# Kernel optimization log

Measured on AMD Instinct MI355X. Metric: run time of the kernel, lower is better.

## Reference

```python
import jax, jax.numpy as jnp
import numpy as np

B, N, D = 64, 4096, 512
ATT = 128


def setup_inputs() -> dict:
    key = jax.random.key(0)
    ks = jax.random.split(key, 7)
    s = lambda fan_in: 1.0 / np.sqrt(fan_in)
    return {
        "v_I": jax.random.normal(ks[0], (B, N, D), dtype=jnp.float32),
        "v_Q": jax.random.normal(ks[1], (B, D), dtype=jnp.float32),
        "W_I": jax.random.normal(ks[2], (D, ATT), dtype=jnp.float32) * s(D),
        "W_Q": jax.random.normal(ks[3], (D, ATT), dtype=jnp.float32) * s(D),
        "b_Q": jnp.zeros((ATT,), dtype=jnp.float32),
        "W_p": jax.random.normal(ks[4], (ATT, 1), dtype=jnp.float32) * s(ATT),
        "b_p": jnp.zeros((1,), dtype=jnp.float32),
    }


def reference(v_I, v_Q, W_I, W_Q, b_Q, W_p, b_p):
    # v_I: [B, N, D], v_Q: [B, D]
    v_I_att = jnp.tanh(jnp.einsum("bnd,da->bna", v_I, W_I))          # [B, N, A]
    v_Q_att = jnp.tanh(v_Q @ W_Q + b_Q)[:, None, :]                  # [B, 1, A]
    h_A = jnp.tanh(v_I_att + v_Q_att)                                # [B, N, A]
    # dropout is identity in inference/reference mode
    p_I = (jnp.einsum("bna,ao->bno", h_A, W_p) + b_p)[..., 0]        # [B, N]
    p_I_output = jax.nn.softmax(p_I, axis=-1)                        # [B, N]
    v_att = jnp.einsum("bn,bnd->bd", p_I_output, v_I)                # [B, D]
    u = v_att + v_Q                                                  # [B, D]
    return (p_I_output, u)
```

## Files before the change

### kernel.cpp

```cpp
#include <hip/hip_runtime.h>
#include <cstdint>
#include <cstddef>

#define B_ 64
#define N_ 4096
#define D_ 512
#define A_ 128
#define BK 64

typedef unsigned short u16;
typedef __attribute__((ext_vector_type(8))) short bf16x8;
typedef __attribute__((ext_vector_type(4))) float f32x4;

__device__ __forceinline__ u16 cvt_bf16(float x) {
    unsigned u = __float_as_uint(x);
    return (u16)((u + 0x7FFFu + ((u >> 16) & 1u)) >> 16);
}
__device__ __forceinline__ unsigned pack2_bf16(float a, float b) {
    unsigned ua = __float_as_uint(a), ub = __float_as_uint(b);
    unsigned ra = (ua + 0x7FFFu + ((ua >> 16) & 1u)) >> 16;
    unsigned rb = (ub + 0x7FFFu + ((ub >> 16) & 1u)) >> 16;
    return ra | (rb << 16);
}
__device__ __forceinline__ float fast_tanh(float x) {
    float ax = fabsf(x);
    float e  = __expf(-2.0f * ax);
    float r  = __fdividef(1.0f - e, 1.0f + e);
    return x < 0.0f ? -r : r;
}
__device__ __forceinline__ void gl_lds16(const void* g, void* l) {
    __builtin_amdgcn_global_load_lds(
        (const __attribute__((address_space(1))) unsigned int*)g,
        (__attribute__((address_space(3))) unsigned int*)l, 16, 0, 0);
}

__global__ void k_prep(const float* __restrict__ WI, const float* __restrict__ vQ,
                       const float* __restrict__ WQ, const float* __restrict__ bQ,
                       u16* __restrict__ Wbf, float* __restrict__ qatt,
                       float* __restrict__ sums, float* __restrict__ u_raw) {
    const int blk = blockIdx.x, t = threadIdx.x;
    if (blk < 64) {
        #pragma unroll
        for (int i = 0; i < 2; ++i) {
            int item = blk * 256 + i * 128 + t;
            int a  = item & 127;
            int d0 = (item >> 7) << 2;
            ushort4 r;
            r.x = cvt_bf16(WI[(d0 + 0) * A_ + a]);
            r.y = cvt_bf16(WI[(d0 + 1) * A_ + a]);
            r.z = cvt_bf16(WI[(d0 + 2) * A_ + a]);
            r.w = cvt_bf16(WI[(d0 + 3) * A_ + a]);
            *(ushort4*)&Wbf[a * D_ + d0] = r;
        }
    } else {
        const int b = blk - 64;
        __shared__ float sq[D_];
        for (int d = t; d < D_; d += 128) sq[d] = vQ[b * D_ + d];
        __syncthreads();
        float acc = bQ[t];
        #pragma unroll 8
        for (int d = 0; d < D_; ++d) acc += sq[d] * WQ[d * A_ + t];
        qatt[b * A_ + t] = fast_tanh(acc);
        float4 z = {0.f, 0.f, 0.f, 0.f};
        *(float4*)(u_raw + b * D_ + t * 4) = z;
        if (t == 0) sums[b] = 0.0f;
    }
}

__global__ void __launch_bounds__(256)
k_fused(const float* __restrict__ vI, const u16* __restrict__ Wbf,
        const float* __restrict__ qatt, const float* __restrict__ Wp,
        float* __restrict__ wbuf, float* __restrict__ sums,
        float* __restrict__ u_raw) {
    const int b  = blockIdx.y;
    const int n0 = blockIdx.x * 128;
    const int t    = threadIdx.x;
    const int lane = t & 63, wave = t >> 6;
    const int l15  = lane & 15, quad = lane >> 4;

    __shared__ float sA[128 * BK];
    __shared__ u16   sB[128 * BK];
    __shared__ float sw[128];
    __shared__ float wred[4];

    f32x4 acc[2][8];
    #pragma unroll
    for (int mt = 0; mt < 2; ++mt)
        #pragma unroll
        for (int nt = 0; nt < 8; ++nt)
            acc[mt][nt] = (f32x4){0.f, 0.f, 0.f, 0.f};

    const float* ga = vI + (size_t)(b * N_ + n0) * D_;

    const int a_row  = wave * 32 + (lane >> 4);
    const float* a_g = ga + (size_t)a_row * D_ + (lane & 15) * 4;
    float* a_l       = sA + (wave * 32) * BK;
    const int b_row  = wave * 32 + (lane >> 3);
    const u16* b_g   = Wbf + (size_t)b_row * D_ + (lane & 7) * 8;
    u16* b_l         = sB + (wave * 32) * BK;

    for (int kr = 0; kr < 8; ++kr) {
        const int k0 = kr * BK;
        #pragma unroll
        for (int c = 0; c < 8; ++c)
            gl_lds16(a_g + c * 4 * D_ + k0, a_l + c * 4 * BK);
        #pragma unroll
        for (int c = 0; c < 4; ++c)
            gl_lds16(b_g + c * 8 * D_ + k0, b_l + c * 8 * BK);
        __syncthreads();
        #pragma unroll
        for (int ks = 0; ks < 2; ++ks) {
            bf16x8 af[2];
            #pragma unroll
            for (int mt = 0; mt < 2; ++mt) {
                const float* ap = sA + (wave * 32 + mt * 16 + l15) * BK + ks * 32 + quad * 8;
                float4 xa = *(const float4*)ap;
                float4 xb = *(const float4*)(ap + 4);
                union { bf16x8 v; unsigned u[4]; } cv;
                cv.u[0] = pack2_bf16(xa.x, xa.y);
                cv.u[1] = pack2_bf16(xa.z, xa.w);
                cv.u[2] = pack2_bf16(xb.x, xb.y);
                cv.u[3] = pack2_bf16(xb.z, xb.w);
                af[mt] = cv.v;
            }
            bf16x8 bfr[8];
            #pragma unroll
            for (int nt = 0; nt < 8; ++nt)
                bfr[nt] = *(const bf16x8*)(sB + (nt * 16 + l15) * BK + ks * 32 + quad * 8);
            #pragma unroll
            for (int mt = 0; mt < 2; ++mt)
                #pragma unroll
                for (int nt = 0; nt < 8; ++nt)
                    acc[mt][nt] = __builtin_amdgcn_mfma_f32_16x16x32_bf16(
                        af[mt], bfr[nt], acc[mt][nt], 0, 0, 0);
        }
        __syncthreads();
    }

    float qa_v[8], wp_v[8];
    #pragma unroll
    for (int nt = 0; nt < 8; ++nt) {
        int a = nt * 16 + l15;
        qa_v[nt] = qatt[b * A_ + a];
        wp_v[nt] = Wp[a];
    }
    float lsum = 0.f;
    #pragma unroll
    for (int mt = 0; mt < 2; ++mt) {
        #pragma unroll
        for (int r = 0; r < 4; ++r) {
            float s = 0.f;
            #pragma unroll
            for (int nt = 0; nt < 8; ++nt) {
                float t1 = fast_tanh(acc[mt][nt][r]);
                float h  = fast_tanh(t1 + qa_v[nt]);
                s += h * wp_v[nt];
            }
            s += __shfl_xor(s, 1, 16);
            s += __shfl_xor(s, 2, 16);
            s += __shfl_xor(s, 4, 16);
            s += __shfl_xor(s, 8, 16);
            float we = __expf(s);
            lsum += we;
            if (l15 == 0) {
                int rloc = wave * 32 + mt * 16 + quad * 4 + r;
                wbuf[(size_t)b * N_ + n0 + rloc] = we;
                sw[rloc] = we;
            }
        }
    }
    lsum += __shfl_xor(lsum, 16, 64);
    lsum += __shfl_xor(lsum, 32, 64);
    if (lane == 0) wred[wave] = lsum;
    __syncthreads();
    if (t == 0) atomicAdd(sums + b, wred[0] + wred[1] + wred[2] + wred[3]);

    const int rr = t >> 7;
    const int c  = t & 127;
    const float4* base = (const float4*)(vI + (size_t)(b * N_ + n0 + rr) * D_) + c;
    float a0 = 0.f, a1 = 0.f, a2 = 0.f, a3 = 0.f;
    #pragma unroll 8
    for (int n = 0; n < 128; n += 2) {
        float4 x = base[n * 128];
        float wn = sw[n + rr];
        a0 += wn * x.x; a1 += wn * x.y; a2 += wn * x.z; a3 += wn * x.w;
    }
    float* ub = u_raw + b * D_ + c * 4;
    atomicAdd(ub + 0, a0);
    atomicAdd(ub + 1, a1);
    atomicAdd(ub + 2, a2);
    atomicAdd(ub + 3, a3);
}

__global__ void __launch_bounds__(256)
k_fin(const float* __restrict__ wbuf, const float* __restrict__ sums,
      const float* __restrict__ u_raw, const float* __restrict__ vQ,
      float* __restrict__ p_out, float* __restrict__ u_out) {
    const int b = blockIdx.x, t = threadIdx.x;
    const float inv = 1.0f / sums[b];
    #pragma unroll
    for (int i = 0; i < 4; ++i) {
        float4 x = *(const float4*)(wbuf + (size_t)b * N_ + i * 1024 + t * 4);
        float4 y = { x.x * inv, x.y * inv, x.z * inv, x.w * inv };
        *(float4*)(p_out + (size_t)b * N_ + i * 1024 + t * 4) = y;
    }
    if (t < 128) {
        float4 ur = *(const float4*)(u_raw + b * D_ + t * 4);
        float4 vq = *(const float4*)(vQ + b * D_ + t * 4);
        float4 o  = { ur.x * inv + vq.x, ur.y * inv + vq.y,
                      ur.z * inv + vq.z, ur.w * inv + vq.w };
        *(float4*)(u_out + b * D_ + t * 4) = o;
    }
}

extern "C" void kernel_launch(void* const* d_in, const int* in_sizes, int n_in,
                              void* d_out, int out_size, void* d_ws, size_t ws_size,
                              hipStream_t stream) {
    const float* vI = (const float*)d_in[0];
    const float* vQ = (const float*)d_in[1];
    const float* WI = (const float*)d_in[2];
    const float* WQ = (const float*)d_in[3];
    const float* bQ = (const float*)d_in[4];
    const float* Wp = (const float*)d_in[5];

    float* out_p = (float*)d_out;
    float* out_u = out_p + (size_t)B_ * N_;

    char* ws = (char*)d_ws;
    u16*   Wbf   = (u16*)ws;
    float* qatt  = (float*)(ws + 131072);
    float* sums  = (float*)(ws + 163840);
    float* u_raw = (float*)(ws + 164864);
    float* wbuf  = (float*)(ws + 295936);

    k_prep<<<128, 128, 0, stream>>>(WI, vQ, WQ, bQ, Wbf, qatt, sums, u_raw);
    k_fused<<<dim3(N_ / 128, B_), 256, 0, stream>>>(vI, Wbf, qatt, Wp,
                                                    wbuf, sums, u_raw);
    k_fin<<<B_, 256, 0, stream>>>(wbuf, sums, u_raw, vQ, out_p, out_u);
}
```

Before: 786.1 us.

## Cache bf16 v_I tile in LDS and reuse it for weighted sum

Restructures the fused kernel to load each 64-row v_I tile once, convert to bf16 into a swizzled LDS buffer covering the full D, and reuse that buffer for the softmax-weighted sum instead of rereading v_I from global memory. W_I is pre-laid out in k_prep so MFMA B fragments load directly from global with register prefetch and manual vmcnt waits. Blocks shrink to 64 rows with 8 waves. This targets halving HBM traffic on v_I, at the cost of bf16 precision in the weighted sum, large LDS use limiting occupancy, and fragile hand-tuned waitcnt counts.

```diff
diff --git a/kernel.cpp b/kernel.cpp
--- a/kernel.cpp
+++ b/kernel.cpp
@@ -6,7 +6,6 @@
 #define N_ 4096
 #define D_ 512
 #define A_ 128
-#define BK 64
 
 typedef unsigned short u16;
 typedef __attribute__((ext_vector_type(8))) short bf16x8;
@@ -22,17 +21,18 @@
     unsigned rb = (ub + 0x7FFFu + ((ub >> 16) & 1u)) >> 16;
     return ra | (rb << 16);
 }
+__device__ __forceinline__ float bf2f(unsigned lo16) {
+    return __uint_as_float(lo16 << 16);
+}
 __device__ __forceinline__ float fast_tanh(float x) {
     float ax = fabsf(x);
     float e  = __expf(-2.0f * ax);
     float r  = __fdividef(1.0f - e, 1.0f + e);
     return x < 0.0f ? -r : r;
 }
-__device__ __forceinline__ void gl_lds16(const void* g, void* l) {
-    __builtin_amdgcn_global_load_lds(
-        (const __attribute__((address_space(1))) unsigned int*)g,
-        (__attribute__((address_space(3))) unsigned int*)l, 16, 0, 0);
-}
+
+#define WAITVM(N) asm volatile("s_waitcnt vmcnt(" #N ")" ::: "memory")
+#define SCHEDB()  __builtin_amdgcn_sched_barrier(0)
 
 __global__ void k_prep(const float* __restrict__ WI, const float* __restrict__ vQ,
                        const float* __restrict__ WQ, const float* __restrict__ bQ,
@@ -50,7 +50,12 @@
             r.y = cvt_bf16(WI[(d0 + 1) * A_ + a]);
             r.z = cvt_bf16(WI[(d0 + 2) * A_ + a]);
             r.w = cvt_bf16(WI[(d0 + 3) * A_ + a]);
-            *(ushort4*)&Wbf[a * D_ + d0] = r;
+            int off = (a >> 4) * 8192
+                    + (d0 >> 5) * 512
+                    + ((d0 >> 3) & 3) * 128
+                    + (a & 15) * 8
+                    + (d0 & 7);
+            *(ushort4*)&Wbf[off] = r;
         }
     } else {
         const int b = blk - 64;
@@ -67,129 +72,155 @@
     }
 }
 
-__global__ void __launch_bounds__(256)
+__global__ void __launch_bounds__(512, 4)
 k_fused(const float* __restrict__ vI, const u16* __restrict__ Wbf,
         const float* __restrict__ qatt, const float* __restrict__ Wp,
         float* __restrict__ wbuf, float* __restrict__ sums,
         float* __restrict__ u_raw) {
     const int b  = blockIdx.y;
-    const int n0 = blockIdx.x * 128;
+    const int n0 = blockIdx.x * 64;
     const int t    = threadIdx.x;
     const int lane = t & 63, wave = t >> 6;
     const int l15  = lane & 15, quad = lane >> 4;
-
-    __shared__ float sA[128 * BK];
-    __shared__ u16   sB[128 * BK];
-    __shared__ float sw[128];
-    __shared__ float wred[4];
-
-    f32x4 acc[2][8];
-    #pragma unroll
-    for (int mt = 0; mt < 2; ++mt)
-        #pragma unroll
-        for (int nt = 0; nt < 8; ++nt)
-            acc[mt][nt] = (f32x4){0.f, 0.f, 0.f, 0.f};
-
-    const float* ga = vI + (size_t)(b * N_ + n0) * D_;
-
-    const int a_row  = wave * 32 + (lane >> 4);
-    const float* a_g = ga + (size_t)a_row * D_ + (lane & 15) * 4;
-    float* a_l       = sA + (wave * 32) * BK;
-    const int b_row  = wave * 32 + (lane >> 3);
-    const u16* b_g   = Wbf + (size_t)b_row * D_ + (lane & 7) * 8;
-    u16* b_l         = sB + (wave * 32) * BK;
-
+    const int rg = wave >> 1, cg = wave & 1;
+
+    __shared__ u16   sA[64 * 512];
+    __shared__ float sred[2][64];
+    __shared__ float sw[64];
+    __shared__ float sph[4][512];
+
+    float qa[4], wp[4];
+    #pragma unroll
+    for (int nt = 0; nt < 4; ++nt) {
+        int a = (cg * 4 + nt) * 16 + l15;
+        qa[nt] = qatt[b * A_ + a];
+        wp[nt] = Wp[a];
+    }
+    SCHEDB();
+
+    const int ar = t >> 3;
+    const int ak = (t & 7) * 8;
+    const float* ag = vI + ((size_t)(b * N_ + n0 + ar) * D_ + ak);
+    char* awb = (char*)sA + ar * 1024 + (((t & 7) * 16) ^ ((ar & 7) << 4));
+
+    const u16* bg = Wbf + lane * 8;
+
+    const int arow = rg * 16 + l15;
+    const char* afb = (const char*)sA + arow * 1024;
+    const int aswz = (arow & 7) << 4;
+
+    f32x4 acc[4];
+    #pragma unroll
+    for (int i = 0; i < 4; ++i) acc[i] = (f32x4){0.f, 0.f, 0.f, 0.f};
+
+    float4 areg[2][2];
+    areg[0][0] = *(const float4*)(ag + 0);
+    areg[0][1] = *(const float4*)(ag + 4);
+    SCHEDB();
+
+    bf16x8 bf0[4], bf1[4];
+
+    #pragma unroll
     for (int kr = 0; kr < 8; ++kr) {
-        const int k0 = kr * BK;
-        #pragma unroll
-        for (int c = 0; c < 8; ++c)
-            gl_lds16(a_g + c * 4 * D_ + k0, a_l + c * 4 * BK);
-        #pragma unroll
-        for (int c = 0; c < 4; ++c)
-            gl_lds16(b_g + c * 8 * D_ + k0, b_l + c * 8 * BK);
-        __syncthreads();
-        #pragma unroll
-        for (int ks = 0; ks < 2; ++ks) {
-            bf16x8 af[2];
+        #pragma unroll
+        for (int nt = 0; nt < 4; ++nt)
+            bf0[nt] = *(const bf16x8*)(bg + ((((cg * 4 + nt) * 16) + kr * 2 + 0) << 9));
+        SCHEDB();
+        #pragma unroll
+        for (int nt = 0; nt < 4; ++nt)
+            bf1[nt] = *(const bf16x8*)(bg + ((((cg * 4 + nt) * 16) + kr * 2 + 1) << 9));
+        SCHEDB();
+        if (kr < 7) {
+            areg[(kr + 1) & 1][0] = *(const float4*)(ag + (kr + 1) * 64);
+            areg[(kr + 1) & 1][1] = *(const float4*)(ag + (kr + 1) * 64 + 4);
+        }
+        SCHEDB();
+
+        if (kr < 7) { WAITVM(10); } else { WAITVM(8); }
+        {
+            float4 x0 = areg[kr & 1][0], x1 = areg[kr & 1][1];
+            union { bf16x8 v; unsigned u[4]; } cv;
+            cv.u[0] = pack2_bf16(x0.x, x0.y);
+            cv.u[1] = pack2_bf16(x0.z, x0.w);
+            cv.u[2] = pack2_bf16(x1.x, x1.y);
+            cv.u[3] = pack2_bf16(x1.z, x1.w);
+            *(bf16x8*)(awb + kr * 128) = cv.v;
+        }
+        SCHEDB();
+        asm volatile("s_waitcnt lgkmcnt(0)" ::: "memory");
+        __builtin_amdgcn_s_barrier();
+        SCHEDB();
+
+        if (kr < 7) { WAITVM(6); } else { WAITVM(4); }
+        {
+            bf16x8 af = *(const bf16x8*)(afb + kr * 128 + ((quad * 16) ^ aswz));
             #pragma unroll
-            for (int mt = 0; mt < 2; ++mt) {
-                const float* ap = sA + (wave * 32 + mt * 16 + l15) * BK + ks * 32 + quad * 8;
-                float4 xa = *(const float4*)ap;
-                float4 xb = *(const float4*)(ap + 4);
-                union { bf16x8 v; unsigned u[4]; } cv;
-                cv.u[0] = pack2_bf16(xa.x, xa.y);
-                cv.u[1] = pack2_bf16(xa.z, xa.w);
-                cv.u[2] = pack2_bf16(xb.x, xb.y);
-                cv.u[3] = pack2_bf16(xb.z, xb.w);
-                af[mt] = cv.v;
-            }
-            bf16x8 bfr[8];
+            for (int nt = 0; nt < 4; ++nt)
+                acc[nt] = __builtin_amdgcn_mfma_f32_16x16x32_bf16(af, bf0[nt], acc[nt], 0, 0, 0);
+        }
+        SCHEDB();
+        if (kr < 7) { WAITVM(2); } else { WAITVM(0); }
+        {
+            bf16x8 af = *(const bf16x8*)(afb + kr * 128 + ((64 + quad * 16) ^ aswz));
             #pragma unroll
-            for (int nt = 0; nt < 8; ++nt)
-                bfr[nt] = *(const bf16x8*)(sB + (nt * 16 + l15) * BK + ks * 32 + quad * 8);
-            #pragma unroll
-            for (int mt = 0; mt < 2; ++mt)
-                #pragma unroll
-                for (int nt = 0; nt < 8; ++nt)
-                    acc[mt][nt] = __builtin_amdgcn_mfma_f32_16x16x32_bf16(
-                        af[mt], bfr[nt], acc[mt][nt], 0, 0, 0);
-        }
-        __syncthreads();
-    }
-
-    float qa_v[8], wp_v[8];
-    #pragma unroll
-    for (int nt = 0; nt < 8; ++nt) {
-        int a = nt * 16 + l15;
-        qa_v[nt] = qatt[b * A_ + a];
-        wp_v[nt] = Wp[a];
-    }
-    float lsum = 0.f;
-    #pragma unroll
-    for (int mt = 0; mt < 2; ++mt) {
-        #pragma unroll
-        for (int r = 0; r < 4; ++r) {
-            float s = 0.f;
-            #pragma unroll
-            for (int nt = 0; nt < 8; ++nt) {
-                float t1 = fast_tanh(acc[mt][nt][r]);
-                float h  = fast_tanh(t1 + qa_v[nt]);
-                s += h * wp_v[nt];
-            }
-            s += __shfl_xor(s, 1, 16);
-            s += __shfl_xor(s, 2, 16);
-            s += __shfl_xor(s, 4, 16);
-            s += __shfl_xor(s, 8, 16);
-            float we = __expf(s);
-            lsum += we;
-            if (l15 == 0) {
-                int rloc = wave * 32 + mt * 16 + quad * 4 + r;
-                wbuf[(size_t)b * N_ + n0 + rloc] = we;
-                sw[rloc] = we;
-            }
-        }
-    }
-    lsum += __shfl_xor(lsum, 16, 64);
-    lsum += __shfl_xor(lsum, 32, 64);
-    if (lane == 0) wred[wave] = lsum;
+            for (int nt = 0; nt < 4; ++nt)
+                acc[nt] = __builtin_amdgcn_mfma_f32_16x16x32_bf16(af, bf1[nt], acc[nt], 0, 0, 0);
+        }
+        SCHEDB();
+    }
+
+    #pragma unroll
+    for (int r = 0; r < 4; ++r) {
+        float s = 0.f;
+        #pragma unroll
+        for (int nt = 0; nt < 4; ++nt) {
+            float t1 = fast_tanh(acc[nt][r]);
+            float h  = fast_tanh(t1 + qa[nt]);
+            s += h * wp[nt];
+        }
+        s += __shfl_xor(s, 1, 16);
+        s += __shfl_xor(s, 2, 16);
+        s += __shfl_xor(s, 4, 16);
+        s += __shfl_xor(s, 8, 16);
+        if (l15 == 0) sred[cg][rg * 16 + quad * 4 + r] = s;
+    }
     __syncthreads();
-    if (t == 0) atomicAdd(sums + b, wred[0] + wred[1] + wred[2] + wred[3]);
-
+    if (t < 64) {
+        float we = __expf(sred[0][t] + sred[1][t]);
+        sw[t] = we;
+        wbuf[(size_t)b * N_ + n0 + t] = we;
+        float ls = we;
+        ls += __shfl_xor(ls, 1);
+        ls += __shfl_xor(ls, 2);
+        ls += __shfl_xor(ls, 4);
+        ls += __shfl_xor(ls, 8);
+        ls += __shfl_xor(ls, 16);
+        ls += __shfl_xor(ls, 32);
+        if (t == 0) atomicAdd(sums + b, ls);
+    }
+    __syncthreads();
+
+    const int dg = t & 127;
     const int rr = t >> 7;
-    const int c  = t & 127;
-    const float4* base = (const float4*)(vI + (size_t)(b * N_ + n0 + rr) * D_) + c;
-    float a0 = 0.f, a1 = 0.f, a2 = 0.f, a3 = 0.f;
-    #pragma unroll 8
-    for (int n = 0; n < 128; n += 2) {
-        float4 x = base[n * 128];
-        float wn = sw[n + rr];
-        a0 += wn * x.x; a1 += wn * x.y; a2 += wn * x.z; a3 += wn * x.w;
-    }
-    float* ub = u_raw + b * D_ + c * 4;
-    atomicAdd(ub + 0, a0);
-    atomicAdd(ub + 1, a1);
-    atomicAdd(ub + 2, a2);
-    atomicAdd(ub + 3, a3);
+    float p0 = 0.f, p1 = 0.f, p2 = 0.f, p3 = 0.f;
+    #pragma unroll
+    for (int i = 0; i < 16; ++i) {
+        int n = i * 4 + rr;
+        const char* src = (const char*)sA + n * 1024 + ((dg * 8) ^ ((n & 7) << 4));
+        uint2 wv = *(const uint2*)src;
+        float wn = sw[n];
+        p0 += wn * bf2f(wv.x & 0xffffu);
+        p1 += wn * bf2f(wv.x >> 16);
+        p2 += wn * bf2f(wv.y & 0xffffu);
+        p3 += wn * bf2f(wv.y >> 16);
+    }
+    *(float4*)&sph[rr][dg * 4] = (float4){p0, p1, p2, p3};
+    __syncthreads();
+    {
+        int d = t;
+        float v = sph[0][d] + sph[1][d] + sph[2][d] + sph[3][d];
+        atomicAdd(u_raw + (size_t)b * D_ + d, v);
+    }
 }
 
 __global__ void __launch_bounds__(256)
@@ -234,7 +265,7 @@
     float* wbuf  = (float*)(ws + 295936);
 
     k_prep<<<128, 128, 0, stream>>>(WI, vQ, WQ, bQ, Wbf, qatt, sums, u_raw);
-    k_fused<<<dim3(N_ / 128, B_), 256, 0, stream>>>(vI, Wbf, qatt, Wp,
-                                                    wbuf, sums, u_raw);
+    k_fused<<<dim3(N_ / 64, B_), 512, 0, stream>>>(vI, Wbf, qatt, Wp,
+                                                   wbuf, sums, u_raw);
     k_fin<<<B_, 256, 0, stream>>>(wbuf, sums, u_raw, vQ, out_p, out_u);
 }
```

Result: faster. 762.6 us (-3.0%).
